# Optimization experiments

Measured on AMD Instinct MI355X. Metric: run time of the kernel, lower is better.

## Reference

```python
import jax, jax.numpy as jnp
import numpy as np

B, TT, TP, TO = 8, 128, 256, 512
V, D, H, L = 1024, 1024, 16, 12
FF = 4 * D
DH = D // H
EPS = 1e-5


def _pe(t, d):
    # sinusoidal PE: concat(sin(omega*t), cos(omega*t)), omega = exp(-ln(1e4)*i/(d/2))
    half = d // 2
    omega = jnp.exp(-jnp.log(10000.0) * jnp.arange(half, dtype=jnp.float32) / half)
    ang = jnp.arange(t, dtype=jnp.float32)[:, None] * omega[None, :]  # (t, d/2)
    return jnp.concatenate([jnp.sin(ang), jnp.cos(ang)], axis=-1)  # (t, d)


def _ln(x, g, b):
    mu = x.mean(axis=-1, keepdims=True)
    var = ((x - mu) ** 2).mean(axis=-1, keepdims=True)
    return (x - mu) / jnp.sqrt(var + EPS) * g + b


def _forward(text_ids, prompt_ids, output_ids, text_tab, prompt_tab, output_tab, sep,
             ln1_g, ln1_b, qkv_w, out_w, out_b, ln2_g, ln2_b,
             ff1_w, ff1_b, ff2_w, ff2_b, fc_w, fc_b):
    emb = lambda ids, tab: tab[ids] + _pe(ids.shape[1], D)[None]
    sep_tok = jnp.broadcast_to(sep, (B, 1, D))
    # join: [text, sep, prompt, sep, output]
    x = jnp.concatenate([emb(text_ids, text_tab), sep_tok,
                         emb(prompt_ids, prompt_tab), sep_tok,
                         emb(output_ids, output_tab)], axis=1)  # (B, T, D)
    T = x.shape[1]
    causal = jnp.tril(jnp.ones((T, T), dtype=bool))  # (T, T)
    scale = DH ** -0.5
    neg = -jnp.finfo(x.dtype).max
    for l in range(L):
        # attention block (prenorm residual); uniform lengths -> mask m is all ones
        h = _ln(x, ln1_g[l], ln1_b[l])
        qkv = h @ qkv_w[l]  # (B, T, 3D)
        q, k, v = jnp.split(qkv, 3, axis=-1)
        q = q.reshape(B, T, H, DH)
        k = k.reshape(B, T, H, DH)
        v = v.reshape(B, T, H, DH)
        e = jnp.einsum('bihd,bjhd->bijh', q, k) * scale
        e = jnp.where(causal[None, :, :, None], e, neg)
        a = jax.nn.softmax(e, axis=2)
        o = jnp.einsum('bijh,bjhd->bihd', a, v).reshape(B, T, D)
        x = x + o @ out_w[l] + out_b[l]
        # ffn block (prenorm residual), exact GELU as torch nn.GELU default
        h2 = _ln(x, ln2_g[l], ln2_b[l])
        ff = jax.nn.gelu(h2 @ ff1_w[l] + ff1_b[l], approximate=False) @ ff2_w[l] + ff2_b[l]
        x = x + ff
    h = x @ fc_w + fc_b  # (B, T, V)
    return h[:, -1, :]  # logits of last position, (B, V)


def setup_inputs() -> dict:
    key = jax.random.key(0)
    ks = iter(jax.random.split(key, 32))
    s = 0.02
    inp = {
        'text_ids': jax.random.randint(next(ks), (B, TT), 0, V),
        'prompt_ids': jax.random.randint(next(ks), (B, TP), 0, V),
        'output_ids': jax.random.randint(next(ks), (B, TO), 0, V),
        'text_tab': jax.random.normal(next(ks), (V, D), jnp.float32) * s,
        'prompt_tab': jax.random.normal(next(ks), (V, D), jnp.float32) * s,
        'output_tab': jax.random.normal(next(ks), (V, D), jnp.float32) * s,
        'sep': jax.random.normal(next(ks), (D,), jnp.float32),
        'ln1_g': jnp.ones((L, D), jnp.float32),
        'ln1_b': jnp.zeros((L, D), jnp.float32),
        'qkv_w': jax.random.normal(next(ks), (L, D, 3 * D), jnp.float32) * s,
        'out_w': jax.random.normal(next(ks), (L, D, D), jnp.float32) * s,
        'out_b': jnp.zeros((L, D), jnp.float32),
        'ln2_g': jnp.ones((L, D), jnp.float32),
        'ln2_b': jnp.zeros((L, D), jnp.float32),
        'ff1_w': jax.random.normal(next(ks), (L, D, FF), jnp.float32) * s,
        'ff1_b': jnp.zeros((L, FF), jnp.float32),
        'ff2_w': jax.random.normal(next(ks), (L, FF, D), jnp.float32) * s,
        'ff2_b': jnp.zeros((L, D), jnp.float32),
        'fc_w': jax.random.normal(next(ks), (D, V), jnp.float32) * s,
        'fc_b': jnp.zeros((V,), jnp.float32),
    }
    return inp


def reference(text_ids, prompt_ids, output_ids, text_tab, prompt_tab, output_tab, sep,
              ln1_g, ln1_b, qkv_w, out_w, out_b, ln2_g, ln2_b,
              ff1_w, ff1_b, ff2_w, ff2_b, fc_w, fc_b):
    return _forward(text_ids, prompt_ids, output_ids, text_tab, prompt_tab, output_tab, sep,
                    ln1_g, ln1_b, qkv_w, out_w, out_b, ln2_g, ln2_b,
                    ff1_w, ff1_b, ff2_w, ff2_b, fc_w, fc_b)
```

## Files before the change

### kernel.cpp

```cpp
#include <hip/hip_runtime.h>
#include <hip/hip_bf16.h>
#include <math.h>

#define Bn 8
#define Tn 898
#define Dn 1024
#define Hn 16
#define DHn 64
#define Ln 12
#define FFn 4096
#define Vn 1024
#define BT (Bn*Tn)
#define MP 7424

typedef short bf16x8 __attribute__((ext_vector_type(8)));
typedef float f32x4 __attribute__((ext_vector_type(4)));

__device__ __forceinline__ ushort f2bf(float f) {
    union { float f; unsigned u; } c; c.f = f;
    unsigned r = c.u + 0x7fffu + ((c.u >> 16) & 1u);
    return (ushort)(r >> 16);
}

__device__ __forceinline__ void glds16(const void* g, void* l) {
    __builtin_amdgcn_global_load_lds(
        (const __attribute__((address_space(1))) unsigned int*)g,
        (__attribute__((address_space(3))) unsigned int*)l, 16, 0, 0);
}

__global__ __launch_bounds__(256) void transpose_cast_kernel(
    const float* __restrict__ in, ushort* __restrict__ out,
    int K, int N, size_t in_ls, size_t out_ls)
{
    __shared__ ushort t[64][68];
    const float* inp = in + (size_t)blockIdx.z * in_ls;
    ushort* outp = out + (size_t)blockIdx.z * out_ls;
    int n0 = blockIdx.x * 64, k0 = blockIdx.y * 64;
    int tx = threadIdx.x & 63, ty = threadIdx.x >> 6;
    #pragma unroll
    for (int p = 0; p < 16; p++) {
        int kl = p * 4 + ty;
        t[tx][kl] = f2bf(inp[(size_t)(k0 + kl) * N + n0 + tx]);
    }
    __syncthreads();
    int tx4 = threadIdx.x & 15, ty4 = threadIdx.x >> 4;
    #pragma unroll
    for (int p = 0; p < 4; p++) {
        int nl = p * 16 + ty4;
        ushort4 v;
        v.x = t[nl][4*tx4]; v.y = t[nl][4*tx4+1]; v.z = t[nl][4*tx4+2]; v.w = t[nl][4*tx4+3];
        *(ushort4*)&outp[(size_t)(n0 + nl) * K + k0 + 4*tx4] = v;
    }
}

__global__ __launch_bounds__(256) void embed_kernel(
    const int* __restrict__ tids, const int* __restrict__ pids, const int* __restrict__ oids,
    const float* __restrict__ ttab, const float* __restrict__ ptab, const float* __restrict__ otab,
    const float* __restrict__ sep, float* __restrict__ x)
{
    int bp = blockIdx.x;
    int b = bp / Tn, pos = bp - b * Tn;
    int d0 = threadIdx.x * 4;
    float4 r;
    if (pos == 128 || pos == 385) {
        r = *(const float4*)(sep + d0);
    } else {
        int t; int id; const float* tab;
        if (pos < 128)      { t = pos;       id = tids[b*128 + t]; tab = ttab; }
        else if (pos < 385) { t = pos - 129; id = pids[b*256 + t]; tab = ptab; }
        else                { t = pos - 386; id = oids[b*512 + t]; tab = otab; }
        float4 e = *(const float4*)(tab + (size_t)id * Dn + d0);
        float pe[4];
        #pragma unroll
        for (int i = 0; i < 4; i++) {
            int d = d0 + i;
            int ii = d & 511;
            float omega = expf(-9.210340371976184f * (float)ii * (1.0f/512.0f));
            float ang = (float)t * omega;
            pe[i] = (d < 512) ? sinf(ang) : cosf(ang);
        }
        r.x = e.x + pe[0]; r.y = e.y + pe[1]; r.z = e.z + pe[2]; r.w = e.w + pe[3];
    }
    *(float4*)(x + (size_t)bp * Dn + d0) = r;
}

__global__ __launch_bounds__(256) void ln_kernel(
    const float* __restrict__ x, const float* __restrict__ g, const float* __restrict__ bt,
    ushort* __restrict__ out)
{
    __shared__ float red[8];
    int row = blockIdx.x, tid = threadIdx.x;
    float4 v = ((const float4*)(x + (size_t)row * Dn))[tid];
    float s = v.x + v.y + v.z + v.w;
    #pragma unroll
    for (int o = 32; o; o >>= 1) s += __shfl_down(s, o);
    if ((tid & 63) == 0) red[tid >> 6] = s;
    __syncthreads();
    float mu = (red[0] + red[1] + red[2] + red[3]) * (1.0f / Dn);
    float d0 = v.x - mu, d1 = v.y - mu, d2 = v.z - mu, d3 = v.w - mu;
    float s2 = d0*d0 + d1*d1 + d2*d2 + d3*d3;
    #pragma unroll
    for (int o = 32; o; o >>= 1) s2 += __shfl_down(s2, o);
    if ((tid & 63) == 0) red[4 + (tid >> 6)] = s2;
    __syncthreads();
    float var = (red[4] + red[5] + red[6] + red[7]) * (1.0f / Dn);
    float rstd = rsqrtf(var + 1e-5f);
    float4 gg = ((const float4*)g)[tid];
    float4 bb = ((const float4*)bt)[tid];
    ushort4 o4;
    o4.x = f2bf(d0 * rstd * gg.x + bb.x);
    o4.y = f2bf(d1 * rstd * gg.y + bb.y);
    o4.z = f2bf(d2 * rstd * gg.z + bb.z);
    o4.w = f2bf(d3 * rstd * gg.w + bb.w);
    ((ushort4*)(out + (size_t)row * Dn))[tid] = o4;
}

template<int BM, int BN, int WM, int WN, int MODE>
__global__ __launch_bounds__(WM*WN*64) void gemm2_kernel(
    const ushort* __restrict__ A, const ushort* __restrict__ Bw,
    const float* __restrict__ bias, const float* __restrict__ resid,
    void* __restrict__ Cout, int M, int N, int K, int nx)
{
    constexpr int NWAVE = WM * WN;
    constexpr int MI = BM / WM / 16;
    constexpr int NI = BN / WN / 16;
    constexpr int GA = (BM / 8) / NWAVE;
    constexpr int GB = (BN / 8) / NWAVE;

    __shared__ ushort sA[2][BM * 64];
    __shared__ ushort sB[2][BN * 64];

    int tid = threadIdx.x, lane = tid & 63, wv = tid >> 6;
    int wm = wv / WN, wn = wv % WN;
    int l16 = lane & 15, lhi = lane >> 4;

    int nb = gridDim.x, bid = blockIdx.x;
    int q = nb >> 3, r = nb & 7;
    int xcd = bid & 7, idx = bid >> 3;
    int wg = (xcd < r ? xcd * (q + 1) : r * (q + 1) + (xcd - r) * q) + idx;
    int mt = wg / nx, ntt = wg - mt * nx;
    int m0 = mt * BM, n0 = ntt * BN;

    f32x4 acc[MI][NI];
    #pragma unroll
    for (int i = 0; i < MI; i++)
        #pragma unroll
        for (int j = 0; j < NI; j++) acc[i][j] = (f32x4){0.f, 0.f, 0.f, 0.f};

    const int sr = lane >> 3;
    const int sc = (lane & 7) * 8;
    const ushort* Ab = A + (size_t)m0 * K + sc;
    const ushort* Bb = Bw + (size_t)n0 * K + sc;

    auto STAGE = [&](int buf, int kk) {
        #pragma unroll
        for (int i = 0; i < GA; i++) {
            int rg = wv * GA + i;
            glds16(Ab + (size_t)(rg * 8 + sr) * K + kk, &sA[buf][rg * 512]);
        }
        #pragma unroll
        for (int i = 0; i < GB; i++) {
            int rg = wv * GB + i;
            glds16(Bb + (size_t)(rg * 8 + sr) * K + kk, &sB[buf][rg * 512]);
        }
    };

    auto COMPUTE = [&](int buf) {
        #pragma unroll
        for (int ks = 0; ks < 2; ks++) {
            bf16x8 af[MI], bfr[NI];
            #pragma unroll
            for (int mi = 0; mi < MI; mi++)
                af[mi] = *(const bf16x8*)&sA[buf][(wm * (16 * MI) + mi * 16 + l16) * 64 + ks * 32 + lhi * 8];
            #pragma unroll
            for (int ni = 0; ni < NI; ni++)
                bfr[ni] = *(const bf16x8*)&sB[buf][(wn * (16 * NI) + ni * 16 + l16) * 64 + ks * 32 + lhi * 8];
            #pragma unroll
            for (int mi = 0; mi < MI; mi++)
                #pragma unroll
                for (int ni = 0; ni < NI; ni++)
                    acc[mi][ni] = __builtin_amdgcn_mfma_f32_16x16x32_bf16(af[mi], bfr[ni], acc[mi][ni], 0, 0, 0);
        }
    };

    int ntile = K >> 6;
    STAGE(0, 0);
    __syncthreads();
    int cur = 0;
    for (int t = 0; t < ntile; t++) {
        if (t + 1 < ntile) STAGE(cur ^ 1, (t + 1) * 64);
        COMPUTE(cur);
        __syncthreads();
        cur ^= 1;
    }

    #pragma unroll
    for (int mi = 0; mi < MI; mi++) {
        int rl = wm * (16 * MI) + mi * 16 + lhi * 4;
        #pragma unroll
        for (int ni = 0; ni < NI; ni++) {
            int gcol = n0 + wn * (16 * NI) + ni * 16 + l16;
            float bs = (MODE == 0) ? 0.0f : bias[gcol];
            #pragma unroll
            for (int j = 0; j < 4; j++) {
                int grow = m0 + rl + j;
                if (grow >= M) continue;
                float v = acc[mi][ni][j] + bs;
                if (MODE == 1) {
                    float rr = resid[(size_t)grow * N + gcol];
                    ((float*)Cout)[(size_t)grow * N + gcol] = rr + v;
                } else if (MODE == 2) {
                    v = 0.5f * v * (1.0f + erff(v * 0.70710678118654752f));
                    ((ushort*)Cout)[(size_t)grow * N + gcol] = f2bf(v);
                } else {
                    ((ushort*)Cout)[(size_t)grow * N + gcol] = f2bf(v);
                }
            }
        }
    }
}

__global__ __launch_bounds__(256) void attn_kernel(
    const ushort* __restrict__ qkv, ushort* __restrict__ out)
{
    __shared__ ushort Ksm[64 * 72];
    __shared__ ushort Vsm[64 * 72];
    __shared__ ushort Psm[4][16 * 72];
    int qt = blockIdx.x, b = blockIdx.y, h = blockIdx.z;
    int tid = threadIdx.x, lane = tid & 63, wave = tid >> 6;
    int l16 = lane & 15, lhi = lane >> 4;

    int qrow = qt*64 + wave*16 + l16;
    bf16x8 qf0 = {}, qf1 = {};
    if (qrow < Tn) {
        const ushort* qp = qkv + (size_t)(b*Tn + qrow) * 3072 + h*64 + lhi*8;
        qf0 = *(const bf16x8*)qp;
        qf1 = *(const bf16x8*)(qp + 32);
    }

    f32x4 o[4];
    #pragma unroll
    for (int i = 0; i < 4; i++) o[i] = (f32x4){0.f,0.f,0.f,0.f};
    float mrun[4] = {-1e30f,-1e30f,-1e30f,-1e30f};
    float sume[4] = {0.f,0.f,0.f,0.f};

    int kr = tid >> 2, cc = (tid & 3) * 16;
    const ushort* kvbase = qkv + (size_t)(b*Tn) * 3072 + h*64 + cc;
    int qg = qt*64 + wave*16 + lhi*4;

    for (int jt = 0; jt <= qt; jt++) {
        int kvr = jt*64 + kr;
        uint4 k0 = make_uint4(0,0,0,0), k1 = k0, v0 = k0, v1 = k0;
        if (kvr < Tn) {
            const ushort* p = kvbase + (size_t)kvr * 3072;
            k0 = *(const uint4*)(p + 1024);
            k1 = *(const uint4*)(p + 1024 + 8);
            v0 = *(const uint4*)(p + 2048);
            v1 = *(const uint4*)(p + 2048 + 8);
        }
        __syncthreads();
        *(uint4*)&Ksm[kr * 72 + cc] = k0;
        *(uint4*)&Ksm[kr * 72 + cc + 8] = k1;
        {
            ushort vv[16];
            *(uint4*)&vv[0] = v0; *(uint4*)&vv[8] = v1;
            #pragma unroll
            for (int i = 0; i < 16; i++) Vsm[(cc + i) * 72 + kr] = vv[i];
        }
        __syncthreads();

        f32x4 s[4];
        #pragma unroll
        for (int ni = 0; ni < 4; ni++) {
            s[ni] = (f32x4){0.f,0.f,0.f,0.f};
            bf16x8 kf0 = *(const bf16x8*)&Ksm[(ni*16 + l16) * 72 + lhi*8];
            bf16x8 kf1 = *(const bf16x8*)&Ksm[(ni*16 + l16) * 72 + lhi*8 + 32];
            s[ni] = __builtin_amdgcn_mfma_f32_16x16x32_bf16(qf0, kf0, s[ni], 0, 0, 0);
            s[ni] = __builtin_amdgcn_mfma_f32_16x16x32_bf16(qf1, kf1, s[ni], 0, 0, 0);
        }

        float pv[4][4];
        #pragma unroll
        for (int j = 0; j < 4; j++) {
            int qgj = qg + j;
            float mx = -1e30f;
            #pragma unroll
            for (int ni = 0; ni < 4; ni++) {
                int kvg = jt*64 + ni*16 + l16;
                float e = (kvg <= qgj && kvg < Tn) ? s[ni][j] * 0.125f : -1e30f;
                pv[ni][j] = e;
                mx = fmaxf(mx, e);
            }
            #pragma unroll
            for (int m = 1; m < 16; m <<= 1) mx = fmaxf(mx, __shfl_xor(mx, m));
            float mnew = fmaxf(mrun[j], mx);
            float fac = expf(mrun[j] - mnew);
            mrun[j] = mnew;
            float rs = 0.f;
            #pragma unroll
            for (int ni = 0; ni < 4; ni++) { pv[ni][j] = expf(pv[ni][j] - mnew); rs += pv[ni][j]; }
            #pragma unroll
            for (int m = 1; m < 16; m <<= 1) rs += __shfl_xor(rs, m);
            sume[j] = sume[j] * fac + rs;
            #pragma unroll
            for (int di = 0; di < 4; di++) o[di][j] *= fac;
        }

        #pragma unroll
        for (int j = 0; j < 4; j++)
            #pragma unroll
            for (int ni = 0; ni < 4; ni++)
                Psm[wave][(lhi*4 + j) * 72 + ni*16 + l16] = f2bf(pv[ni][j]);
        __syncthreads();

        bf16x8 pf0 = *(const bf16x8*)&Psm[wave][l16 * 72 + lhi*8];
        bf16x8 pf1 = *(const bf16x8*)&Psm[wave][l16 * 72 + lhi*8 + 32];
        #pragma unroll
        for (int di = 0; di < 4; di++) {
            bf16x8 vf0 = *(const bf16x8*)&Vsm[(di*16 + l16) * 72 + lhi*8];
            bf16x8 vf1 = *(const bf16x8*)&Vsm[(di*16 + l16) * 72 + lhi*8 + 32];
            o[di] = __builtin_amdgcn_mfma_f32_16x16x32_bf16(pf0, vf0, o[di], 0, 0, 0);
            o[di] = __builtin_amdgcn_mfma_f32_16x16x32_bf16(pf1, vf1, o[di], 0, 0, 0);
        }
    }

    #pragma unroll
    for (int j = 0; j < 4; j++) {
        int qgj = qg + j;
        if (qgj >= Tn) continue;
        float inv = 1.0f / sume[j];
        #pragma unroll
        for (int di = 0; di < 4; di++)
            out[(size_t)(b*Tn + qgj) * Dn + h*64 + di*16 + l16] = f2bf(o[di][j] * inv);
    }
}

__global__ __launch_bounds__(256) void fc_kernel(
    const float* __restrict__ x, const float* __restrict__ w,
    const float* __restrict__ bias, float* __restrict__ out)
{
    __shared__ float xs[Dn];
    int b = blockIdx.y;
    int v = blockIdx.x * 256 + threadIdx.x;
    float4 t = ((const float4*)(x + (size_t)(b*Tn + Tn - 1) * Dn))[threadIdx.x];
    ((float4*)xs)[threadIdx.x] = t;
    __syncthreads();
    float acc = bias[v];
    for (int d = 0; d < Dn; d++)
        acc = fmaf(xs[d], w[(size_t)d * Vn + v], acc);
    out[(size_t)b * Vn + v] = acc;
}

extern "C" void kernel_launch(void* const* d_in, const int* in_sizes, int n_in,
                              void* d_out, int out_size, void* d_ws, size_t ws_size,
                              hipStream_t stream)
{
    const int*   text_ids  = (const int*)d_in[0];
    const int*   prompt_ids= (const int*)d_in[1];
    const int*   output_ids= (const int*)d_in[2];
    const float* text_tab  = (const float*)d_in[3];
    const float* prompt_tab= (const float*)d_in[4];
    const float* output_tab= (const float*)d_in[5];
    const float* sep       = (const float*)d_in[6];
    const float* ln1_g     = (const float*)d_in[7];
    const float* ln1_b     = (const float*)d_in[8];
    const float* qkv_w     = (const float*)d_in[9];
    const float* out_w     = (const float*)d_in[10];
    const float* out_b     = (const float*)d_in[11];
    const float* ln2_g     = (const float*)d_in[12];
    const float* ln2_b     = (const float*)d_in[13];
    const float* ff1_w     = (const float*)d_in[14];
    const float* ff1_b     = (const float*)d_in[15];
    const float* ff2_w     = (const float*)d_in[16];
    const float* ff2_b     = (const float*)d_in[17];
    const float* fc_w      = (const float*)d_in[18];
    const float* fc_b      = (const float*)d_in[19];

    char* ws = (char*)d_ws;
    float*  x    = (float*)(ws);
    ushort* h    = (ushort*)(ws + 29425664);
    ushort* qkv  = (ushort*)(ws + 44630016);
    ushort* attn = (ushort*)(ws + 90243072);
    ushort* ff1o = (ushort*)(ws + 105447424);
    ushort* wT   = (ushort*)(ws + 166264832);

    const size_t L_STRIDE = 12582912;
    const size_t OFF_QKV = 0, OFF_OUT = 3145728, OFF_FF1 = 4194304, OFF_FF2 = 8388608;
    const size_t upfront_need = 166264832ULL + 2ULL * L_STRIDE * Ln;
    const bool upfront = ws_size >= upfront_need;

    if (upfront) {
        transpose_cast_kernel<<<dim3(48,16,Ln), 256, 0, stream>>>(qkv_w, wT + OFF_QKV, Dn, 3*Dn, (size_t)Dn*3*Dn, L_STRIDE);
        transpose_cast_kernel<<<dim3(16,16,Ln), 256, 0, stream>>>(out_w, wT + OFF_OUT, Dn, Dn,   (size_t)Dn*Dn,   L_STRIDE);
        transpose_cast_kernel<<<dim3(64,16,Ln), 256, 0, stream>>>(ff1_w, wT + OFF_FF1, Dn, FFn,  (size_t)Dn*FFn,  L_STRIDE);
        transpose_cast_kernel<<<dim3(16,64,Ln), 256, 0, stream>>>(ff2_w, wT + OFF_FF2, FFn, Dn,  (size_t)FFn*Dn,  L_STRIDE);
    }

    embed_kernel<<<BT, 256, 0, stream>>>(text_ids, prompt_ids, output_ids,
                                         text_tab, prompt_tab, output_tab, sep, x);

    for (int l = 0; l < Ln; l++) {
        ushort* wb = upfront ? (wT + (size_t)l * L_STRIDE) : wT;
        if (!upfront) {
            transpose_cast_kernel<<<dim3(48,16,1), 256, 0, stream>>>(qkv_w + (size_t)l*Dn*3*Dn, wb + OFF_QKV, Dn, 3*Dn, 0, 0);
            transpose_cast_kernel<<<dim3(16,16,1), 256, 0, stream>>>(out_w + (size_t)l*Dn*Dn,   wb + OFF_OUT, Dn, Dn,   0, 0);
            transpose_cast_kernel<<<dim3(64,16,1), 256, 0, stream>>>(ff1_w + (size_t)l*Dn*FFn,  wb + OFF_FF1, Dn, FFn,  0, 0);
            transpose_cast_kernel<<<dim3(16,64,1), 256, 0, stream>>>(ff2_w + (size_t)l*FFn*Dn,  wb + OFF_FF2, FFn, Dn,  0, 0);
        }
        ln_kernel<<<BT, 256, 0, stream>>>(x, ln1_g + l*Dn, ln1_b + l*Dn, h);
        gemm2_kernel<256,256,2,4,0><<<12*29, 512, 0, stream>>>(
            h, wb + OFF_QKV, nullptr, nullptr, qkv, BT, 3*Dn, Dn, 12);
        attn_kernel<<<dim3(15, Bn, Hn), 256, 0, stream>>>(qkv, attn);
        gemm2_kernel<128,128,2,2,1><<<8*57, 256, 0, stream>>>(
            attn, wb + OFF_OUT, out_b + l*Dn, x, x, BT, Dn, Dn, 8);
        ln_kernel<<<BT, 256, 0, stream>>>(x, ln2_g + l*Dn, ln2_b + l*Dn, h);
        gemm2_kernel<256,256,2,4,2><<<16*29, 512, 0, stream>>>(
            h, wb + OFF_FF1, ff1_b + l*FFn, nullptr, ff1o, BT, FFn, Dn, 16);
        gemm2_kernel<128,128,2,2,1><<<8*57, 256, 0, stream>>>(
            ff1o, wb + OFF_FF2, ff2_b + l*Dn, x, x, BT, Dn, FFn, 8);
    }

    fc_kernel<<<dim3(Vn/256, Bn), 256, 0, stream>>>(x, fc_w, fc_b, (float*)d_out);
}
```

Baseline: 6.158 ms.

## Rewrite GEMM with swizzled LDS, split-phase staging and priority-scheduled MFMA

Replaces the double-buffered GEMM with an 8-wave kernel that splits each K-tile into four quadrant MFMA phases. Global-to-LDS loads for the next B tile and the A tile two steps ahead are interleaved between phases, with explicit vmcnt waits and raised wave priority around the MFMA blocks. LDS rows are XOR-swizzled to avoid bank conflicts. The output-projection and FF2 GEMMs move from 128x128 tiles with 4 waves to 256x128 tiles with 8 waves, giving fewer, larger blocks. The main risks are the hand-written barrier and vmcnt ordering, and lower occupancy from the larger tiles.

New measurement: 5.936 ms. -3.6%, faster.

```diff
diff --git a/kernel.cpp b/kernel.cpp
--- a/kernel.cpp
+++ b/kernel.cpp
@@ -27,6 +27,11 @@
         (const __attribute__((address_space(1))) unsigned int*)g,
         (__attribute__((address_space(3))) unsigned int*)l, 16, 0, 0);
 }
+
+#define BARRIER() __builtin_amdgcn_s_barrier()
+#define VMCNT4() asm volatile("s_waitcnt vmcnt(4)" ::: "memory")
+#define VMCNT0() asm volatile("s_waitcnt vmcnt(0)" ::: "memory")
+#define SETPRIO(p) __builtin_amdgcn_s_setprio(p)
 
 __global__ __launch_bounds__(256) void transpose_cast_kernel(
     const float* __restrict__ in, ushort* __restrict__ out,
@@ -116,28 +121,29 @@
 }
 
 template<int BM, int BN, int WM, int WN, int MODE>
-__global__ __launch_bounds__(WM*WN*64) void gemm2_kernel(
+__global__ __launch_bounds__(512, 2) void gemm8_kernel(
     const ushort* __restrict__ A, const ushort* __restrict__ Bw,
     const float* __restrict__ bias, const float* __restrict__ resid,
     void* __restrict__ Cout, int M, int N, int K, int nx)
 {
-    constexpr int NWAVE = WM * WN;
     constexpr int MI = BM / WM / 16;
     constexpr int NI = BN / WN / 16;
-    constexpr int GA = (BM / 8) / NWAVE;
-    constexpr int GB = (BN / 8) / NWAVE;
-
-    __shared__ ushort sA[2][BM * 64];
-    __shared__ ushort sB[2][BN * 64];
+    constexpr int MH = MI / 2, NH = NI / 2;
+    constexpr int GA = BM / 128;
+    constexpr int GB = BN / 128;
+    constexpr int RA = BM / 2, RB = BN / 2;
+
+    __shared__ ushort sA0[BM * 64], sB0[BN * 64];
+    __shared__ ushort sA1[BM * 64], sB1[BN * 64];
 
     int tid = threadIdx.x, lane = tid & 63, wv = tid >> 6;
     int wm = wv / WN, wn = wv % WN;
     int l16 = lane & 15, lhi = lane >> 4;
 
     int nb = gridDim.x, bid = blockIdx.x;
-    int q = nb >> 3, r = nb & 7;
+    int qq = nb >> 3, rr8 = nb & 7;
     int xcd = bid & 7, idx = bid >> 3;
-    int wg = (xcd < r ? xcd * (q + 1) : r * (q + 1) + (xcd - r) * q) + idx;
+    int wg = (xcd < rr8 ? xcd * (qq + 1) : rr8 * (qq + 1) + (xcd - rr8) * qq) + idx;
     int mt = wg / nx, ntt = wg - mt * nx;
     int m0 = mt * BM, n0 = ntt * BN;
 
@@ -147,59 +153,111 @@
         #pragma unroll
         for (int j = 0; j < NI; j++) acc[i][j] = (f32x4){0.f, 0.f, 0.f, 0.f};
 
-    const int sr = lane >> 3;
-    const int sc = (lane & 7) * 8;
-    const ushort* Ab = A + (size_t)m0 * K + sc;
-    const ushort* Bb = Bw + (size_t)n0 * K + sc;
-
-    auto STAGE = [&](int buf, int kk) {
-        #pragma unroll
-        for (int i = 0; i < GA; i++) {
-            int rg = wv * GA + i;
-            glds16(Ab + (size_t)(rg * 8 + sr) * K + kk, &sA[buf][rg * 512]);
-        }
-        #pragma unroll
-        for (int i = 0; i < GB; i++) {
-            int rg = wv * GB + i;
-            glds16(Bb + (size_t)(rg * 8 + sr) * K + kk, &sB[buf][rg * 512]);
-        }
-    };
-
-    auto COMPUTE = [&](int buf) {
-        #pragma unroll
-        for (int ks = 0; ks < 2; ks++) {
-            bf16x8 af[MI], bfr[NI];
-            #pragma unroll
-            for (int mi = 0; mi < MI; mi++)
-                af[mi] = *(const bf16x8*)&sA[buf][(wm * (16 * MI) + mi * 16 + l16) * 64 + ks * 32 + lhi * 8];
-            #pragma unroll
-            for (int ni = 0; ni < NI; ni++)
-                bfr[ni] = *(const bf16x8*)&sB[buf][(wn * (16 * NI) + ni * 16 + l16) * 64 + ks * 32 + lhi * 8];
-            #pragma unroll
-            for (int mi = 0; mi < MI; mi++)
+    int srow = lane >> 3;
+    int schk = (lane & 7) ^ srow;
+    const char* Abase = (const char*)A + (size_t)m0 * K * 2 + schk * 16;
+    const char* Bbase = (const char*)Bw + (size_t)n0 * K * 2 + schk * 16;
+
+    auto stageA = [&](ushort* dst, int t2) {
+        size_t ko = (size_t)t2 * 128;
+        #pragma unroll
+        for (int h = 0; h < 2; h++)
+            #pragma unroll
+            for (int j = 0; j < GA; j++) {
+                int rrow = h * RA + wv * (RA / 8) + j * 8;
+                glds16(Abase + (size_t)(rrow + srow) * (K * 2) + ko, dst + rrow * 64);
+            }
+    };
+    auto stageB = [&](ushort* dst, int h, int t1) {
+        size_t ko = (size_t)t1 * 128;
+        #pragma unroll
+        for (int j = 0; j < GB; j++) {
+            int rrow = h * RB + wv * (RB / 8) + j * 8;
+            glds16(Bbase + (size_t)(rrow + srow) * (K * 2) + ko, dst + rrow * 64);
+        }
+    };
+
+    int rbA = wm * (MI * 16) + l16;
+    int rbB = wn * (NI * 16) + l16;
+    int sc0 = ((lhi) ^ (l16 & 7)) * 8;
+    int sc1 = ((4 + lhi) ^ (l16 & 7)) * 8;
+
+    bf16x8 af[MH][2], bf0[NH][2], bf1[NH][2];
+
+    auto ldA = [&](const ushort* S, int mh) {
+        #pragma unroll
+        for (int mi = 0; mi < MH; mi++) {
+            int row = rbA + (mh * MH + mi) * 16;
+            af[mi][0] = *(const bf16x8*)&S[row * 64 + sc0];
+            af[mi][1] = *(const bf16x8*)&S[row * 64 + sc1];
+        }
+    };
+    auto ldB = [&](bf16x8 (&bf)[NH][2], const ushort* S, int nh) {
+        #pragma unroll
+        for (int ni = 0; ni < NH; ni++) {
+            int row = rbB + (nh * NH + ni) * 16;
+            bf[ni][0] = *(const bf16x8*)&S[row * 64 + sc0];
+            bf[ni][1] = *(const bf16x8*)&S[row * 64 + sc1];
+        }
+    };
+    auto MM = [&](int mh, int nh, bf16x8 (&bf)[NH][2]) {
+        #pragma unroll
+        for (int ks = 0; ks < 2; ks++)
+            #pragma unroll
+            for (int mi = 0; mi < MH; mi++)
                 #pragma unroll
-                for (int ni = 0; ni < NI; ni++)
-                    acc[mi][ni] = __builtin_amdgcn_mfma_f32_16x16x32_bf16(af[mi], bfr[ni], acc[mi][ni], 0, 0, 0);
-        }
+                for (int ni = 0; ni < NH; ni++)
+                    acc[mh*MH+mi][nh*NH+ni] = __builtin_amdgcn_mfma_f32_16x16x32_bf16(
+                        af[mi][ks], bf[ni][ks], acc[mh*MH+mi][nh*NH+ni], 0, 0, 0);
     };
 
     int ntile = K >> 6;
-    STAGE(0, 0);
-    __syncthreads();
-    int cur = 0;
-    for (int t = 0; t < ntile; t++) {
-        if (t + 1 < ntile) STAGE(cur ^ 1, (t + 1) * 64);
-        COMPUTE(cur);
-        __syncthreads();
-        cur ^= 1;
+
+    auto tile = [&](const ushort* AS, const ushort* BS, ushort* ASw, ushort* BSo, int t) {
+        bool sb = (t + 1) < ntile;
+        bool sa = (t + 2) < ntile;
+        ldA(AS, 0); ldB(bf0, BS, 0);
+        if (sb) stageB(BSo, 0, t + 1);
+        BARRIER();
+        SETPRIO(1); MM(0, 0, bf0); SETPRIO(0);
+        BARRIER();
+        ldB(bf1, BS, 1);
+        if (sb) stageB(BSo, 1, t + 1);
+        BARRIER();
+        SETPRIO(1); MM(0, 1, bf1); SETPRIO(0);
+        BARRIER();
+        ldA(AS, 1);
+        BARRIER();
+        SETPRIO(1); MM(1, 1, bf1); SETPRIO(0);
+        BARRIER();
+        if (sa) {
+            stageA(ASw, t + 2);
+            SETPRIO(1); MM(1, 0, bf0); SETPRIO(0);
+            VMCNT4();
+        } else {
+            SETPRIO(1); MM(1, 0, bf0); SETPRIO(0);
+            VMCNT0();
+        }
+        BARRIER();
+    };
+
+    stageA(sA0, 0);
+    stageB(sB0, 0, 0); stageB(sB0, 1, 0);
+    if (ntile > 1) stageA(sA1, 1);
+    VMCNT4();
+    BARRIER();
+
+    for (int t = 0; t < ntile; t += 2) {
+        tile(sA0, sB0, sA0, sB1, t);
+        tile(sA1, sB1, sA1, sB0, t + 1);
     }
 
     #pragma unroll
     for (int mi = 0; mi < MI; mi++) {
-        int rl = wm * (16 * MI) + mi * 16 + lhi * 4;
+        int rl = wm * (MI * 16) + mi * 16 + lhi * 4;
         #pragma unroll
         for (int ni = 0; ni < NI; ni++) {
-            int gcol = n0 + wn * (16 * NI) + ni * 16 + l16;
+            int gcol = n0 + wn * (NI * 16) + ni * 16 + l16;
             float bs = (MODE == 0) ? 0.0f : bias[gcol];
             #pragma unroll
             for (int j = 0; j < 4; j++) {
@@ -207,8 +265,8 @@
                 if (grow >= M) continue;
                 float v = acc[mi][ni][j] + bs;
                 if (MODE == 1) {
-                    float rr = resid[(size_t)grow * N + gcol];
-                    ((float*)Cout)[(size_t)grow * N + gcol] = rr + v;
+                    float rv = resid[(size_t)grow * N + gcol];
+                    ((float*)Cout)[(size_t)grow * N + gcol] = rv + v;
                 } else if (MODE == 2) {
                     v = 0.5f * v * (1.0f + erff(v * 0.70710678118654752f));
                     ((ushort*)Cout)[(size_t)grow * N + gcol] = f2bf(v);
@@ -408,15 +466,15 @@
             transpose_cast_kernel<<<dim3(16,64,1), 256, 0, stream>>>(ff2_w + (size_t)l*FFn*Dn,  wb + OFF_FF2, FFn, Dn,  0, 0);
         }
         ln_kernel<<<BT, 256, 0, stream>>>(x, ln1_g + l*Dn, ln1_b + l*Dn, h);
-        gemm2_kernel<256,256,2,4,0><<<12*29, 512, 0, stream>>>(
+        gemm8_kernel<256,256,2,4,0><<<29*12, 512, 0, stream>>>(
             h, wb + OFF_QKV, nullptr, nullptr, qkv, BT, 3*Dn, Dn, 12);
         attn_kernel<<<dim3(15, Bn, Hn), 256, 0, stream>>>(qkv, attn);
-        gemm2_kernel<128,128,2,2,1><<<8*57, 256, 0, stream>>>(
+        gemm8_kernel<256,128,4,2,1><<<29*8, 512, 0, stream>>>(
             attn, wb + OFF_OUT, out_b + l*Dn, x, x, BT, Dn, Dn, 8);
         ln_kernel<<<BT, 256, 0, stream>>>(x, ln2_g + l*Dn, ln2_b + l*Dn, h);
-        gemm2_kernel<256,256,2,4,2><<<16*29, 512, 0, stream>>>(
+        gemm8_kernel<256,256,2,4,2><<<29*16, 512, 0, stream>>>(
             h, wb + OFF_FF1, ff1_b + l*FFn, nullptr, ff1o, BT, FFn, Dn, 16);
-        gemm2_kernel<128,128,2,2,1><<<8*57, 256, 0, stream>>>(
+        gemm8_kernel<256,128,4,2,1><<<29*8, 512, 0, stream>>>(
             ff1o, wb + OFF_FF2, ff2_b + l*Dn, x, x, BT, Dn, FFn, 8);
     }
 
```
